# Kernel optimization log

Hardware: AMD Instinct MI355X
Metric: run time of the kernel (lower is better)

Reference implementation:

```python
import jax, jax.numpy as jnp
import numpy as np

N, E = 100000, 1600000          # nodes, edges
DIN, DH, DOUT = 128, 128, 64    # input_dim, hidden_dim, output_dim


def setup_inputs() -> dict:
    key = jax.random.key(0)
    k0, k1, k2, k3 = jax.random.split(key, 4)
    x = jax.random.normal(k0, (N, DIN), dtype=jnp.float32)
    edge_index = jax.random.randint(k1, (2, E), 0, N)
    # GCNConv params (glorot-ish weights, zero bias)
    W1 = jax.random.normal(k2, (DIN, DH), dtype=jnp.float32) / np.sqrt(DIN).astype(np.float32)
    b1 = jnp.zeros((DH,), jnp.float32)
    W2 = jax.random.normal(k3, (DH, DOUT), dtype=jnp.float32) / np.sqrt(DH).astype(np.float32)
    b2 = jnp.zeros((DOUT,), jnp.float32)
    return {"x": x, "edge_index": edge_index, "W1": W1, "b1": b1, "W2": W2, "b2": b2}


def _gcn_conv(h_in, W, b, src, dst, norm_e, self_norm, n):
    # PyG GCNConv: transform, then normalized sum-aggregation with self-loops.
    h = h_in @ W                                   # [N, dout]
    msg = h[src] * norm_e[:, None]                 # [E, dout] gather + edge scale
    agg = jax.ops.segment_sum(msg, dst, num_segments=n)
    agg = agg + h * self_norm[:, None]             # self-loop contribution (norm = 1/deg)
    return agg + b


def reference(x, edge_index, W1, b1, W2, b2):
    src, dst = edge_index[0], edge_index[1]
    n = x.shape[0]
    # degree including self-loop, computed on dst (PyG convention)
    deg = jax.ops.segment_sum(jnp.ones((src.shape[0],), x.dtype), dst, num_segments=n) + 1.0
    dinv = jax.lax.rsqrt(deg)
    norm_e = dinv[src] * dinv[dst]                 # per-edge D^-1/2 A D^-1/2
    self_norm = dinv * dinv
    h = _gcn_conv(x, W1, b1, src, dst, norm_e, self_norm, n)
    h = jax.nn.relu(h)                             # dropout is identity in eval mode
    out = _gcn_conv(h, W2, b2, src, dst, norm_e, self_norm, n)
    return out
```

## Files before the change

### kernel.cpp

```cpp
#include <hip/hip_runtime.h>

#define NN 100000
#define NE 1600000
#define NBUCK 1563
#define NBH 256
#define CHUNK 6250
#define NSEG 8
#define SEGC (NBH/NSEG)
#define NBXB 12500
#define NBG 1563
#define NBGG 512


typedef short bf16x8 __attribute__((ext_vector_type(8)));
typedef float f32x4  __attribute__((ext_vector_type(4)));
typedef float f32x2  __attribute__((ext_vector_type(2)));

__device__ __forceinline__ float b2f(unsigned short u) {
    return __uint_as_float(((unsigned int)u) << 16);
}
__device__ __forceinline__ unsigned short f2b(float f) {
    unsigned int x = __float_as_uint(f);
    x += 0x7FFFu + ((x >> 16) & 1u);
    return (unsigned short)(x >> 16);
}

__global__ __launch_bounds__(256) void k_pre(const float* __restrict__ x,
                                             unsigned short* __restrict__ xb,
                                             const int* __restrict__ dst,
                                             int* __restrict__ ghist) {
    int b = blockIdx.x;
    if (b < NBXB) {
        int id = b * 256 + threadIdx.x;
        float4 v = ((const float4*)x)[id];
        ushort4 o;
        o.x = f2b(v.x); o.y = f2b(v.y); o.z = f2b(v.z); o.w = f2b(v.w);
        ((ushort4*)xb)[id] = o;
        return;
    }
    __shared__ int h[NBUCK];
    int tid = threadIdx.x;
    int i = b - NBXB;
    for (int k = tid; k < NBUCK; k += 256) h[k] = 0;
    __syncthreads();
    int e0 = i * CHUNK;
    for (int e = e0 + tid; e < e0 + CHUNK; e += 256) {
        unsigned d = (unsigned)dst[e];
        if (d < NN) atomicAdd(&h[d >> 6], 1);
    }
    __syncthreads();
    for (int k = tid; k < NBUCK; k += 256) ghist[i * NBUCK + k] = h[k];
}

__global__ __launch_bounds__(256) void k_scanB(const int* __restrict__ ghist,
                                               int* __restrict__ boffT,
                                               int* __restrict__ tot) {
    __shared__ int part[NSEG][32];
    int kk = threadIdx.x & 31, seg = threadIdx.x >> 5;
    int k = blockIdx.x * 32 + kk;
    bool ok = (k < NBUCK);
    int i0 = seg * SEGC;
    int S = 0;
    if (ok) {
#pragma unroll 8
        for (int i = i0; i < i0 + SEGC; ++i) S += ghist[i * NBUCK + k];
    }
    part[seg][kk] = S;
    __syncthreads();
    int pre = 0;
#pragma unroll
    for (int s2 = 0; s2 < NSEG; ++s2) pre += (s2 < seg) ? part[s2][kk] : 0;
    if (ok) {
        int run = pre;
#pragma unroll 8
        for (int i = i0; i < i0 + SEGC; ++i) {
            int c = ghist[i * NBUCK + k];
            boffT[i * NBUCK + k] = run;
            run += c;
        }
        if (seg == NSEG - 1) tot[k] = run;
    }
}

__global__ __launch_bounds__(256) void k_place(const int* __restrict__ src,
                                               const int* __restrict__ dst,
                                               const int* __restrict__ tot,
                                               const int* __restrict__ boffT,
                                               int* __restrict__ ebuf,
                                               int* __restrict__ bbase_out) {
    __shared__ int cur[NBUCK];
    __shared__ int s[256];
    const int tid = threadIdx.x, bid = blockIdx.x;
    const int i = ((bid & 7) * (NBH / 8)) + (bid >> 3);
    int k0 = tid * 7;
    int v[7]; int S = 0;
#pragma unroll
    for (int q = 0; q < 7; ++q) {
        int k = k0 + q;
        v[q] = (k < NBUCK) ? tot[k] : 0;
        S += v[q];
    }
    s[tid] = S;
    __syncthreads();
    for (int off = 1; off < 256; off <<= 1) {
        int t = (tid >= off) ? s[tid - off] : 0;
        __syncthreads();
        s[tid] += t;
        __syncthreads();
    }
    int run = s[tid] - S;
#pragma unroll
    for (int q = 0; q < 7; ++q) {
        int k = k0 + q;
        if (k < NBUCK) {
            cur[k] = run + boffT[i * NBUCK + k];
            if (bid == 0) bbase_out[k] = run;
            run += v[q];
        }
    }
    __syncthreads();
    int e0 = i * CHUNK;
    for (int e = e0 + tid; e < e0 + CHUNK; e += 256) {
        unsigned d = (unsigned)dst[e];
        if (d >= NN) continue;
        unsigned sv = (unsigned)src[e];
        if (sv >= NN) sv = 0;
        int pos = atomicAdd(&cur[d >> 6], 1);
        ebuf[pos] = (int)(sv | ((d & 63u) << 17));
    }
}

__global__ __launch_bounds__(256) void k_binC(const int* __restrict__ bbase,
                                              const int* __restrict__ tot,
                                              const int* __restrict__ ebuf,
                                              int* __restrict__ row_start,
                                              float* __restrict__ dinv,
                                              int* __restrict__ csr) {
    __shared__ int cnt[64], excl[64], cur[64];
    int b = blockIdx.x, tid = threadIdx.x;
    int n0 = b * 64;
    int base = bbase[b], end = base + tot[b];
    if (tid < 64) cnt[tid] = 0;
    __syncthreads();
    for (int i = base + tid; i < end; i += 256)
        atomicAdd(&cnt[((unsigned)ebuf[i]) >> 17], 1);
    __syncthreads();
    if (tid == 0) {
        int run = 0;
        for (int t = 0; t < 64; ++t) { excl[t] = run; run += cnt[t]; }
    }
    __syncthreads();
    if (tid < 64) {
        int node = n0 + tid;
        if (node < NN) {
            row_start[node] = base + excl[tid];
            dinv[node] = rsqrtf((float)cnt[tid] + 1.0f);
        }
        cur[tid] = base + excl[tid];
    }
    if (b == NBUCK - 1 && tid == 0) row_start[NN] = end;
    __syncthreads();
    for (int i = base + tid; i < end; i += 256) {
        unsigned rec = (unsigned)ebuf[i];
        int pos = atomicAdd(&cur[rec >> 17], 1);
        csr[pos] = (int)(rec & 0x1FFFFu);
    }
}

__global__ __launch_bounds__(256) void k_agg1(const unsigned short* __restrict__ xb,
                                              const float* __restrict__ dinv,
                                              const int* __restrict__ row_start,
                                              const int* __restrict__ csr,
                                              char* __restrict__ P) {
    int node = blockIdx.x * 4 + (threadIdx.x >> 6);
    int lane = threadIdx.x & 63;
    int sub  = lane >> 4;
    int dimb = lane & 15;
    const uint4* X4 = (const uint4*)xb;
    float dv = dinv[node];
    float sn4 = dv * dv * 0.25f;
    uint4 sv = X4[(size_t)node * 16 + dimb];
    f32x2 a0, a1, a2, a3;
    a0.x = __uint_as_float(sv.x << 16) * sn4;  a0.y = __uint_as_float(sv.x & 0xFFFF0000u) * sn4;
    a1.x = __uint_as_float(sv.y << 16) * sn4;  a1.y = __uint_as_float(sv.y & 0xFFFF0000u) * sn4;
    a2.x = __uint_as_float(sv.z << 16) * sn4;  a2.y = __uint_as_float(sv.z & 0xFFFF0000u) * sn4;
    a3.x = __uint_as_float(sv.w << 16) * sn4;  a3.y = __uint_as_float(sv.w & 0xFFFF0000u) * sn4;
    int base = row_start[node], end = row_start[node + 1];
    for (int c0 = base; c0 < end; c0 += 64) {
        int idx = c0 + lane;
        int cl = min(idx, end - 1);
        int s = csr[cl];
        float wv = (idx < end) ? dinv[s] * dv : 0.f;
        int ng = min(64, end - c0);
        for (int g = 0; g * 4 < ng; ++g) {
            int   sq = __shfl(s,  g * 4 + sub);
            float wq = __shfl(wv, g * 4 + sub);
            uint4 v = X4[(size_t)sq * 16 + dimb];
            f32x2 wv2; wv2.x = wq; wv2.y = wq;
            f32x2 xv;
            xv.x = __uint_as_float(v.x << 16); xv.y = __uint_as_float(v.x & 0xFFFF0000u);
            a0 = __builtin_elementwise_fma(xv, wv2, a0);
            xv.x = __uint_as_float(v.y << 16); xv.y = __uint_as_float(v.y & 0xFFFF0000u);
            a1 = __builtin_elementwise_fma(xv, wv2, a1);
            xv.x = __uint_as_float(v.z << 16); xv.y = __uint_as_float(v.z & 0xFFFF0000u);
            a2 = __builtin_elementwise_fma(xv, wv2, a2);
            xv.x = __uint_as_float(v.w << 16); xv.y = __uint_as_float(v.w & 0xFFFF0000u);
            a3 = __builtin_elementwise_fma(xv, wv2, a3);
        }
    }
#pragma unroll
    for (int mgap = 16; mgap < 64; mgap <<= 1) {
        a0.x += __shfl_xor(a0.x, mgap); a0.y += __shfl_xor(a0.y, mgap);
        a1.x += __shfl_xor(a1.x, mgap); a1.y += __shfl_xor(a1.y, mgap);
        a2.x += __shfl_xor(a2.x, mgap); a2.y += __shfl_xor(a2.y, mgap);
        a3.x += __shfl_xor(a3.x, mgap); a3.y += __shfl_xor(a3.y, mgap);
    }
    if (lane < 16) {
        uint4 o;
        o.x = (unsigned)f2b(a0.x) | ((unsigned)f2b(a0.y) << 16);
        o.y = (unsigned)f2b(a1.x) | ((unsigned)f2b(a1.y) << 16);
        o.z = (unsigned)f2b(a2.x) | ((unsigned)f2b(a2.y) << 16);
        o.w = (unsigned)f2b(a3.x) | ((unsigned)f2b(a3.y) << 16);
        ((uint4*)(P + (size_t)node * 256))[lane] = o;
    }
}

__global__ __launch_bounds__(256) void k_gemm12(const float* __restrict__ W1,
                                                const float* __restrict__ b1,
                                                const float* __restrict__ W2,
                                                char* __restrict__ P) {
    __shared__ short Wl1[16384];
    __shared__ short Wl2[8192];
    __shared__ __align__(16) short Cl[4][16][136];
    const int tid = threadIdx.x;
    const int w = tid >> 6, lane = tid & 63;
    const int quad = lane >> 4, l15 = lane & 15;

    for (int i = tid; i < 16384; i += 256) {
        int j = i & 7, l = (i >> 3) & 63, ks = (i >> 9) & 3, ct = i >> 11;
        int k = ks * 32 + ((l >> 4) << 3) + j;
        int c = ct * 16 + (l & 15);
        Wl1[i] = (short)f2b(W1[k * 128 + c]);
    }
    for (int i = tid; i < 8192; i += 256) {
        int j = i & 7, l = (i >> 3) & 63, ks = (i >> 9) & 3, ct = i >> 11;
        int k = ks * 32 + ((l >> 4) << 3) + j;
        int c = ct * 16 + (l & 15);
        Wl2[i] = (short)f2b(W2[k * 64 + c]);
    }
    float bias1[8];
#pragma unroll
    for (int ct = 0; ct < 8; ++ct) bias1[ct] = b1[ct * 16 + l15];
    __syncthreads();

    for (int t = blockIdx.x; t < NBG; t += NBGG) {
        const int r0 = t * 64;
        const int m = r0 + w * 16 + l15;
        const bool mok = (m < NN);
        bf16x8 a[4];
#pragma unroll
        for (int ks = 0; ks < 4; ++ks) {
            if (mok) a[ks] = *(const bf16x8*)(P + (size_t)m * 256 + (ks * 32 + quad * 8) * 2);
            else     a[ks] = bf16x8{0,0,0,0,0,0,0,0};
        }
#pragma unroll
        for (int ct = 0; ct < 8; ++ct) {
            f32x4 c = {0.f, 0.f, 0.f, 0.f};
#pragma unroll
            for (int ks = 0; ks < 4; ++ks) {
                bf16x8 b = *(const bf16x8*)&Wl1[((ct * 4 + ks) * 64 + lane) * 8];
                c = __builtin_amdgcn_mfma_f32_16x16x32_bf16(a[ks], b, c, 0, 0, 0);
            }
#pragma unroll
            for (int r = 0; r < 4; ++r)
                Cl[w][quad * 4 + r][ct * 16 + l15] =
                    (short)f2b(fmaxf(c[r] + bias1[ct], 0.f));
        }
        __syncthreads();
        bf16x8 a2[4];
#pragma unroll
        for (int ks = 0; ks < 4; ++ks)
            a2[ks] = *(const bf16x8*)&Cl[w][l15][ks * 32 + quad * 8];
#pragma unroll
        for (int ct = 0; ct < 4; ++ct) {
            f32x4 c = {0.f, 0.f, 0.f, 0.f};
#pragma unroll
            for (int ks = 0; ks < 4; ++ks) {
                bf16x8 b = *(const bf16x8*)&Wl2[((ct * 4 + ks) * 64 + lane) * 8];
                c = __builtin_amdgcn_mfma_f32_16x16x32_bf16(a2[ks], b, c, 0, 0, 0);
            }
#pragma unroll
            for (int r = 0; r < 4; ++r) {
                int node = r0 + w * 16 + quad * 4 + r;
                if (node < NN)
                    *(unsigned short*)(P + (size_t)node * 256 + (ct * 16 + l15) * 2) =
                        f2b(c[r]);
            }
        }
        __syncthreads();
    }
}

__global__ __launch_bounds__(256) void k_agg2(const float* __restrict__ dinv,
                                              const int* __restrict__ row_start,
                                              const int* __restrict__ csr,
                                              const char* __restrict__ P,
                                              const float* __restrict__ b2,
                                              float* __restrict__ outp) {
    int node = blockIdx.x * 4 + (threadIdx.x >> 6);
    int lane = threadIdx.x & 63;
    int sub  = lane >> 3;
    int dimb = lane & 7;
    const uint4* P4 = (const uint4*)P;
    float dv = dinv[node];
    float sn8 = dv * dv * 0.125f;
    uint4 sv = P4[(size_t)node * 16 + dimb];
    f32x2 a0, a1, a2, a3;
    a0.x = __uint_as_float(sv.x << 16) * sn8;  a0.y = __uint_as_float(sv.x & 0xFFFF0000u) * sn8;
    a1.x = __uint_as_float(sv.y << 16) * sn8;  a1.y = __uint_as_float(sv.y & 0xFFFF0000u) * sn8;
    a2.x = __uint_as_float(sv.z << 16) * sn8;  a2.y = __uint_as_float(sv.z & 0xFFFF0000u) * sn8;
    a3.x = __uint_as_float(sv.w << 16) * sn8;  a3.y = __uint_as_float(sv.w & 0xFFFF0000u) * sn8;
    int base = row_start[node], end = row_start[node + 1];
    if (end > base) {
        for (int c0 = base; c0 < end; c0 += 64) {
            int idx = c0 + lane;
            int cl = min(idx, end - 1);
            int s = csr[cl];
            float wv = (idx < end) ? dinv[s] * dv : 0.f;
            int ng = min(64, end - c0);
            for (int g = 0; g * 8 < ng; ++g) {
                int   sq = __shfl(s,  g * 8 + sub);
                float wq = __shfl(wv, g * 8 + sub);
                uint4 v = P4[(size_t)sq * 16 + dimb];
                f32x2 wv2; wv2.x = wq; wv2.y = wq;
                f32x2 xv;
                xv.x = __uint_as_float(v.x << 16); xv.y = __uint_as_float(v.x & 0xFFFF0000u);
                a0 = __builtin_elementwise_fma(xv, wv2, a0);
                xv.x = __uint_as_float(v.y << 16); xv.y = __uint_as_float(v.y & 0xFFFF0000u);
                a1 = __builtin_elementwise_fma(xv, wv2, a1);
                xv.x = __uint_as_float(v.z << 16); xv.y = __uint_as_float(v.z & 0xFFFF0000u);
                a2 = __builtin_elementwise_fma(xv, wv2, a2);
                xv.x = __uint_as_float(v.w << 16); xv.y = __uint_as_float(v.w & 0xFFFF0000u);
                a3 = __builtin_elementwise_fma(xv, wv2, a3);
            }
        }
    }
#pragma unroll
    for (int mgap = 8; mgap < 64; mgap <<= 1) {
        a0.x += __shfl_xor(a0.x, mgap); a0.y += __shfl_xor(a0.y, mgap);
        a1.x += __shfl_xor(a1.x, mgap); a1.y += __shfl_xor(a1.y, mgap);
        a2.x += __shfl_xor(a2.x, mgap); a2.y += __shfl_xor(a2.y, mgap);
        a3.x += __shfl_xor(a3.x, mgap); a3.y += __shfl_xor(a3.y, mgap);
    }
    if (lane < 8) {
        float4 ba = ((const float4*)b2)[lane * 2];
        float4 bb = ((const float4*)b2)[lane * 2 + 1];
        float4 o0, o1;
        o0.x = a0.x + ba.x; o0.y = a0.y + ba.y; o0.z = a1.x + ba.z; o0.w = a1.y + ba.w;
        o1.x = a2.x + bb.x; o1.y = a2.y + bb.y; o1.z = a3.x + bb.z; o1.w = a3.y + bb.w;
        ((float4*)outp)[(size_t)node * 16 + lane * 2]     = o0;
        ((float4*)outp)[(size_t)node * 16 + lane * 2 + 1] = o1;
    }
}

extern "C" void kernel_launch(void* const* d_in, const int* in_sizes, int n_in,
                              void* d_out, int out_size, void* d_ws, size_t ws_size,
                              hipStream_t stream) {
    const float* x  = (const float*)d_in[0];
    const int*   ei = (const int*)d_in[1];
    const float* W1 = (const float*)d_in[2];
    const float* b1 = (const float*)d_in[3];
    const float* W2 = (const float*)d_in[4];
    const float* b2 = (const float*)d_in[5];
    float* out = (float*)d_out;
    const int* src = ei;
    const int* dst = ei + NE;

    char* ws = (char*)d_ws;
    unsigned short* xb        = (unsigned short*)(ws + 0);
    char*           P         = ws + 25600000;
    int*            ghist     = (int*)(ws + 25600000);
    int*            boffT     = (int*)(ws + 27200512);
    int*            tot       = (int*)(ws + 28801024);
    int*            bbase     = (int*)(ws + 28807276);
    int*            row_start = (int*)(ws + 51200000);
    float*          dinv      = (float*)(ws + 51600004);
    int*            csr       = (int*)(ws + 52000004);
    int*            ebuf      = (int*)(ws + 58400004);

    k_pre  <<<NBXB + NBH, 256, 0, stream>>>(x, xb, dst, ghist);
    k_scanB<<<(NBUCK + 31) / 32, 256, 0, stream>>>(ghist, boffT, tot);
    k_place<<<NBH, 256, 0, stream>>>(src, dst, tot, boffT, ebuf, bbase);
    k_binC <<<NBUCK, 256, 0, stream>>>(bbase, tot, ebuf, row_start, dinv, csr);

    k_agg1  <<<NN / 4, 256, 0, stream>>>(xb, dinv, row_start, csr, P);
    k_gemm12<<<NBGG, 256, 0, stream>>>(W1, b1, W2, P);
    k_agg2  <<<NN / 4, 256, 0, stream>>>(dinv, row_start, csr, P, b2, out);
}
```

Measured before the change: 293.1 us.

## Split fused GEMM into two kernels and compact layer-2 features to 64-wide rows

The fused two-GEMM kernel becomes two separate kernels. The hidden activations go through a global bf16 buffer H instead of shared memory, and the second GEMM writes a dense 64-column T2 buffer rather than the first half of 256-byte P rows. The aim is to halve the row stride k_agg2 gathers over, giving better cache-line use for the random neighbour reads, and to drop the in-loop syncthreads. The cost is an extra kernel launch and an extra 25 MB round-trip of H through global memory. The grid size is also doubled.

```diff
diff --git a/kernel.cpp b/kernel.cpp
--- a/kernel.cpp
+++ b/kernel.cpp
@@ -9,7 +9,7 @@
 #define SEGC (NBH/NSEG)
 #define NBXB 12500
 #define NBG 1563
-#define NBGG 512
+#define NBGG 1024
 
 
 typedef short bf16x8 __attribute__((ext_vector_type(8)));
@@ -225,13 +225,11 @@
     }
 }
 
-__global__ __launch_bounds__(256) void k_gemm12(const float* __restrict__ W1,
-                                                const float* __restrict__ b1,
-                                                const float* __restrict__ W2,
-                                                char* __restrict__ P) {
+__global__ __launch_bounds__(256) void k_g1(const char* __restrict__ P,
+                                            const float* __restrict__ W1,
+                                            const float* __restrict__ b1,
+                                            unsigned short* __restrict__ H) {
     __shared__ short Wl1[16384];
-    __shared__ short Wl2[8192];
-    __shared__ __align__(16) short Cl[4][16][136];
     const int tid = threadIdx.x;
     const int w = tid >> 6, lane = tid & 63;
     const int quad = lane >> 4, l15 = lane & 15;
@@ -242,45 +240,66 @@
         int c = ct * 16 + (l & 15);
         Wl1[i] = (short)f2b(W1[k * 128 + c]);
     }
+    float bias1[8];
+#pragma unroll
+    for (int ct = 0; ct < 8; ++ct) bias1[ct] = b1[ct * 16 + l15];
+    __syncthreads();
+
+    for (int t = blockIdx.x; t < NBG; t += NBGG) {
+        const int r0 = t * 64;
+        const int m = r0 + w * 16 + l15;
+        const bool mok = (m < NN);
+        bf16x8 a[4];
+#pragma unroll
+        for (int ks = 0; ks < 4; ++ks) {
+            if (mok) a[ks] = *(const bf16x8*)(P + (size_t)m * 256 + (ks * 32 + quad * 8) * 2);
+            else     a[ks] = bf16x8{0,0,0,0,0,0,0,0};
+        }
+#pragma unroll
+        for (int ct = 0; ct < 8; ++ct) {
+            f32x4 c = {0.f, 0.f, 0.f, 0.f};
+#pragma unroll
+            for (int ks = 0; ks < 4; ++ks) {
+                bf16x8 b = *(const bf16x8*)&Wl1[((ct * 4 + ks) * 64 + lane) * 8];
+                c = __builtin_amdgcn_mfma_f32_16x16x32_bf16(a[ks], b, c, 0, 0, 0);
+            }
+#pragma unroll
+            for (int r = 0; r < 4; ++r) {
+                int row = r0 + w * 16 + quad * 4 + r;
+                if (row < NN)
+                    H[(size_t)row * 128 + ct * 16 + l15] =
+                        (unsigned short)f2b(fmaxf(c[r] + bias1[ct], 0.f));
+            }
+        }
+    }
+}
+
+__global__ __launch_bounds__(256) void k_g2(const unsigned short* __restrict__ H,
+                                            const float* __restrict__ W2,
+                                            unsigned short* __restrict__ T2) {
+    __shared__ short Wl2[8192];
+    const int tid = threadIdx.x;
+    const int w = tid >> 6, lane = tid & 63;
+    const int quad = lane >> 4, l15 = lane & 15;
+
     for (int i = tid; i < 8192; i += 256) {
         int j = i & 7, l = (i >> 3) & 63, ks = (i >> 9) & 3, ct = i >> 11;
         int k = ks * 32 + ((l >> 4) << 3) + j;
         int c = ct * 16 + (l & 15);
         Wl2[i] = (short)f2b(W2[k * 64 + c]);
     }
-    float bias1[8];
-#pragma unroll
-    for (int ct = 0; ct < 8; ++ct) bias1[ct] = b1[ct * 16 + l15];
     __syncthreads();
 
     for (int t = blockIdx.x; t < NBG; t += NBGG) {
         const int r0 = t * 64;
         const int m = r0 + w * 16 + l15;
         const bool mok = (m < NN);
-        bf16x8 a[4];
+        bf16x8 a2[4];
 #pragma unroll
         for (int ks = 0; ks < 4; ++ks) {
-            if (mok) a[ks] = *(const bf16x8*)(P + (size_t)m * 256 + (ks * 32 + quad * 8) * 2);
-            else     a[ks] = bf16x8{0,0,0,0,0,0,0,0};
-        }
-#pragma unroll
-        for (int ct = 0; ct < 8; ++ct) {
-            f32x4 c = {0.f, 0.f, 0.f, 0.f};
-#pragma unroll
-            for (int ks = 0; ks < 4; ++ks) {
-                bf16x8 b = *(const bf16x8*)&Wl1[((ct * 4 + ks) * 64 + lane) * 8];
-                c = __builtin_amdgcn_mfma_f32_16x16x32_bf16(a[ks], b, c, 0, 0, 0);
-            }
-#pragma unroll
-            for (int r = 0; r < 4; ++r)
-                Cl[w][quad * 4 + r][ct * 16 + l15] =
-                    (short)f2b(fmaxf(c[r] + bias1[ct], 0.f));
-        }
-        __syncthreads();
-        bf16x8 a2[4];
-#pragma unroll
-        for (int ks = 0; ks < 4; ++ks)
-            a2[ks] = *(const bf16x8*)&Cl[w][l15][ks * 32 + quad * 8];
+            if (mok) a2[ks] = *(const bf16x8*)&H[(size_t)m * 128 + ks * 32 + quad * 8];
+            else     a2[ks] = bf16x8{0,0,0,0,0,0,0,0};
+        }
 #pragma unroll
         for (int ct = 0; ct < 4; ++ct) {
             f32x4 c = {0.f, 0.f, 0.f, 0.f};
@@ -293,28 +312,26 @@
             for (int r = 0; r < 4; ++r) {
                 int node = r0 + w * 16 + quad * 4 + r;
                 if (node < NN)
-                    *(unsigned short*)(P + (size_t)node * 256 + (ct * 16 + l15) * 2) =
-                        f2b(c[r]);
+                    T2[(size_t)node * 64 + ct * 16 + l15] = (unsigned short)f2b(c[r]);
             }
         }
-        __syncthreads();
     }
 }
 
 __global__ __launch_bounds__(256) void k_agg2(const float* __restrict__ dinv,
                                               const int* __restrict__ row_start,
                                               const int* __restrict__ csr,
-                                              const char* __restrict__ P,
+                                              const unsigned short* __restrict__ T2,
                                               const float* __restrict__ b2,
                                               float* __restrict__ outp) {
     int node = blockIdx.x * 4 + (threadIdx.x >> 6);
     int lane = threadIdx.x & 63;
     int sub  = lane >> 3;
     int dimb = lane & 7;
-    const uint4* P4 = (const uint4*)P;
+    const uint4* T4 = (const uint4*)T2;
     float dv = dinv[node];
     float sn8 = dv * dv * 0.125f;
-    uint4 sv = P4[(size_t)node * 16 + dimb];
+    uint4 sv = T4[(size_t)node * 8 + dimb];
     f32x2 a0, a1, a2, a3;
     a0.x = __uint_as_float(sv.x << 16) * sn8;  a0.y = __uint_as_float(sv.x & 0xFFFF0000u) * sn8;
     a1.x = __uint_as_float(sv.y << 16) * sn8;  a1.y = __uint_as_float(sv.y & 0xFFFF0000u) * sn8;
@@ -331,7 +348,7 @@
             for (int g = 0; g * 8 < ng; ++g) {
                 int   sq = __shfl(s,  g * 8 + sub);
                 float wq = __shfl(wv, g * 8 + sub);
-                uint4 v = P4[(size_t)sq * 16 + dimb];
+                uint4 v = T4[(size_t)sq * 8 + dimb];
                 f32x2 wv2; wv2.x = wq; wv2.y = wq;
                 f32x2 xv;
                 xv.x = __uint_as_float(v.x << 16); xv.y = __uint_as_float(v.x & 0xFFFF0000u);
@@ -378,7 +395,9 @@
 
     char* ws = (char*)d_ws;
     unsigned short* xb        = (unsigned short*)(ws + 0);
+    unsigned short* H         = (unsigned short*)(ws + 0);
     char*           P         = ws + 25600000;
+    unsigned short* T2        = (unsigned short*)(ws + 25600000);
     int*            ghist     = (int*)(ws + 25600000);
     int*            boffT     = (int*)(ws + 27200512);
     int*            tot       = (int*)(ws + 28801024);
@@ -393,7 +412,8 @@
     k_place<<<NBH, 256, 0, stream>>>(src, dst, tot, boffT, ebuf, bbase);
     k_binC <<<NBUCK, 256, 0, stream>>>(bbase, tot, ebuf, row_start, dinv, csr);
 
-    k_agg1  <<<NN / 4, 256, 0, stream>>>(xb, dinv, row_start, csr, P);
-    k_gemm12<<<NBGG, 256, 0, stream>>>(W1, b1, W2, P);
-    k_agg2  <<<NN / 4, 256, 0, stream>>>(dinv, row_start, csr, P, b2, out);
-}
+    k_agg1<<<NN / 4, 256, 0, stream>>>(xb, dinv, row_start, csr, P);
+    k_g1  <<<NBGG, 256, 0, stream>>>(P, W1, b1, H);
+    k_g2  <<<NBGG, 256, 0, stream>>>(H, W2, T2);
+    k_agg2<<<NN / 4, 256, 0, stream>>>(dinv, row_start, csr, T2, b2, out);
+}
```

Measured after the change: 309.9 us. 1.06x slower.
